# Kernel tuning notes

Hardware: AMD Instinct MI355X
Metric: run time of the kernel (lower is better)

## Reference

```python
import jax, jax.numpy as jnp
import numpy as np

jax.config.update("jax_enable_x64", True)  # int64 coordinate hashes (scaling up to 1e15)

N_IN, N_OUT = 64, 32
NP_, NG = 200000, 400000

# Same coordinate hash as the original module: columns [batch, x, y, z]
_SCALE = jnp.array([1, 10 ** 5, 10 ** 10, 10 ** 15], dtype=jnp.int64)
# 27 kernel offsets of the 3x3x3 generative transpose conv (output-stride units)
_OFF3 = np.array([[i, j, k] for i in (-1, 0, 1) for j in (-1, 0, 1) for k in (-1, 0, 1)], dtype=np.int64)
_OFF4 = jnp.asarray(np.concatenate([np.zeros((27, 1), np.int64), _OFF3], axis=1))  # batch offset = 0


def _hash(c):
    return (c.astype(jnp.int64) * _SCALE).sum(-1)


def setup_inputs() -> dict:
    rng = np.random.default_rng(0)
    G = 128  # stride-2 lattice: input coords are even, in [0, 256)
    lin = rng.choice(G ** 3, size=NP_, replace=False)  # unique voxels
    xs, ys, zs = lin % G, (lin // G) % G, lin // (G * G)
    in_coords = np.stack([np.zeros(NP_, np.int64), 2 * xs, 2 * ys, 2 * zs], axis=1)
    # guide (occupied) coords: input coords shifted by random kernel offsets -> mostly hits
    guide_coords = np.concatenate([in_coords, in_coords], axis=0).copy()
    guide_coords[:, 1:] += _OFF3[rng.integers(0, 27, size=NG)]
    key = jax.random.key(0)
    k1, k2, k3 = jax.random.split(key, 3)
    in_feats = jax.random.normal(k1, (NP_, N_IN), dtype=jnp.float32)
    weights = (jax.random.normal(k2, (27, N_IN, N_OUT), dtype=jnp.float32) / float(np.sqrt(27 * N_IN))).astype(jnp.float32)
    bias = (jax.random.normal(k3, (N_OUT,), dtype=jnp.float32) * 0.01).astype(jnp.float32)
    return {"in_feats": in_feats, "weights": weights, "bias": bias,
            "in_coords": jnp.asarray(in_coords), "guide_coords": jnp.asarray(guide_coords)}


def _forward(in_feats, weights, bias, in_coords, guide_coords):
    # Hash-table over input coordinates (sort + binary search == isin with index)
    in_keys = _hash(in_coords)                # [Np]
    order = jnp.argsort(in_keys)
    skeys = in_keys[order]
    n = skeys.shape[0]
    # Generative transpose conv: output q gets contribution from input p when q = p + off,
    # i.e. p = q - off. Pruning keeps only outputs coinciding with guide coords, so we
    # evaluate the conv directly at the guide coordinates and mask non-generated rows.
    p_keys = _hash(guide_coords[None, :, :] - _OFF4[:, None, :])   # [27, Ng]
    pos = jnp.clip(jnp.searchsorted(skeys, p_keys), 0, n - 1)
    found = skeys[pos] == p_keys                                   # [27, Ng] bool
    idx = order[pos]                                               # [27, Ng]

    def step(acc, xs):
        i, f, w = xs
        g = in_feats[i] * f[:, None].astype(in_feats.dtype)        # [Ng, N_in] gather + mask
        return acc + g @ w, None                                   # small GEMM per offset

    acc0 = jnp.zeros((guide_coords.shape[0], weights.shape[-1]), in_feats.dtype)
    acc, _ = jax.lax.scan(step, acc0, (idx, found, weights))
    exists = found.any(axis=0)                                     # generated-set membership
    return (acc + bias.astype(acc.dtype)) * exists[:, None].astype(acc.dtype)


def reference(in_feats, weights, bias, in_coords, guide_coords):
    return _forward(in_feats, weights, bias, in_coords, guide_coords)
```

## Files before the change

kernel.cpp:

```cpp
#include <hip/hip_runtime.h>

#define NIN 64
#define NOUT 32
#define TBITS 21
#define TSIZE (1 << TBITS)
#define NB 512
#define CHUNK 4096
#define KPT (CHUNK / 256)
#define BLKG 128

typedef __attribute__((ext_vector_type(8))) short short8;
typedef __attribute__((ext_vector_type(4))) float float4v;
typedef __attribute__((ext_vector_type(4))) unsigned short ushort4v;

__device__ __forceinline__ unsigned short bf16rne(float x) {
    unsigned u = __float_as_uint(x);
    u += 0x7fffu + ((u >> 16) & 1u);
    return (unsigned short)(u >> 16);
}

__device__ __forceinline__ int bucket_of(int4 q, int* cls) {
    int c = (q.y & 1) | ((q.z & 1) << 1) | ((q.w & 1) << 2);
    *cls = c;
    int sp = ((q.y >> 6) & 3) | (((q.z >> 6) & 3) << 2) | (((q.w >> 6) & 3) << 4);
    return (c << 6) | sp;
}

__global__ void prep(int4* __restrict__ ws4, int n4,
                     int4* __restrict__ count4,
                     const float* __restrict__ w, unsigned short* __restrict__ wt,
                     const float* __restrict__ f, unsigned short* __restrict__ fb,
                     int fn4) {
    int i = blockIdx.x * blockDim.x + threadIdx.x;
    if (i < n4) ws4[i] = make_int4(-1, -1, -1, -1);
    if (i < NB / 4) count4[i] = make_int4(0, 0, 0, 0);
    if (i < 27 * 64 * 32) {
        int oi = i >> 11;
        int k  = (i >> 5) & 63;
        int ch = i & 31;
        wt[oi * 2048 + ch * 64 + k] = bf16rne(w[i]);
    }
    if (i < fn4) {
        float4 v = ((const float4*)f)[i];
        ushort4v o;
        o.x = bf16rne(v.x); o.y = bf16rne(v.y);
        o.z = bf16rne(v.z); o.w = bf16rne(v.w);
        ((ushort4v*)fb)[i] = o;
    }
}

__global__ void bc(const int* __restrict__ coords, int np, int* __restrict__ table,
                   const int* __restrict__ guide, int ng, int* __restrict__ count) {
    __shared__ int hist[NB];
    for (int i = threadIdx.x; i < NB; i += blockDim.x) hist[i] = 0;
    int gi = blockIdx.x * blockDim.x + threadIdx.x;
    if (gi < np) {
        int x = coords[gi * 4 + 1];
        int y = coords[gi * 4 + 2];
        int z = coords[gi * 4 + 3];
        table[(x >> 1) | ((y >> 1) << 7) | ((z >> 1) << 14)] = gi;
    }
    __syncthreads();
    int base = blockIdx.x * CHUNK;
    if (base < ng) {
        int end = base + CHUNK; if (end > ng) end = ng;
        for (int i = base + threadIdx.x; i < end; i += blockDim.x) {
            int c;
            int b = bucket_of(((const int4*)guide)[i], &c);
            atomicAdd(&hist[b], 1);
        }
        __syncthreads();
        for (int i = threadIdx.x; i < NB; i += blockDim.x)
            if (hist[i]) atomicAdd(&count[i], hist[i]);
    }
}

__global__ void scanB(const int* __restrict__ count, int* __restrict__ cursor,
                      int* __restrict__ classbase) {
    __shared__ int ps[512];
    __shared__ int cb[9];
    int t = threadIdx.x;
    int v = count[t];
    ps[t] = v;
    __syncthreads();
    #pragma unroll
    for (int off = 1; off < 512; off <<= 1) {
        int val = ps[t];
        int u = (t >= off) ? ps[t - off] : 0;
        __syncthreads();
        ps[t] = val + u;
        __syncthreads();
    }
    int incl = ps[t];
    if (t == 0) {
        int base = 0;
        #pragma unroll
        for (int cc = 0; cc < 8; ++cc) {
            cb[cc] = base;
            int hi = ps[cc * 64 + 63];
            int lo = cc ? ps[cc * 64 - 1] : 0;
            base += (hi - lo + BLKG - 1) & ~(BLKG - 1);
        }
        cb[8] = base;
        for (int j = 0; j < 9; ++j) classbase[j] = cb[j];
    }
    __syncthreads();
    int cc = t >> 6;
    int lo = cc ? ps[cc * 64 - 1] : 0;
    cursor[t] = cb[cc] + (incl - v) - lo;
}

__global__ void scat(const int* __restrict__ guide, int ng,
                     int* __restrict__ cursor, int2* __restrict__ sorted) {
    __shared__ int hist[NB];
    int t = threadIdx.x;
    for (int i = t; i < NB; i += 256) hist[i] = 0;
    __syncthreads();
    int base = blockIdx.x * CHUNK;
    int packed[KPT];
    int ey[KPT];
    #pragma unroll
    for (int k = 0; k < KPT; ++k) {
        int i = base + k * 256 + t;
        packed[k] = -1;
        ey[k] = 0;
        if (i < ng) {
            int4 q = ((const int4*)guide)[i];
            int c;
            int b = bucket_of(q, &c);
            int lr = atomicAdd(&hist[b], 1);
            packed[k] = (b << 13) | lr;
            ey[k] = (q.y + 1) | ((q.z + 1) << 9) | ((q.w + 1) << 18);
        }
    }
    __syncthreads();
    for (int i = t; i < NB; i += 256) {
        int h = hist[i];
        hist[i] = h ? atomicAdd(&cursor[i], h) : 0;
    }
    __syncthreads();
    #pragma unroll
    for (int k = 0; k < KPT; ++k) {
        if (packed[k] >= 0) {
            int b  = packed[k] >> 13;
            int lr = packed[k] & 8191;
            int i  = base + k * 256 + t;
            int2 e;
            e.x = i | ((b >> 6) << 24);
            e.y = ey[k];
            sorted[hist[b] + lr] = e;
        }
    }
}


template<int C>
__device__ __forceinline__ void probe2t(const int* __restrict__ table, int2 s2,
                                        int quad, int* o0, int* o1) {
    int qx = (s2.y & 511) - 1;
    int qy = ((s2.y >> 9) & 511) - 1;
    int qz = ((s2.y >> 18) & 511) - 1;
    int res[2];
    #pragma unroll
    for (int r = 0; r < 2; ++r) {
        int sub = quad + r * 4;
        int offx = (C & 1) ? ((sub & 1) ? 1 : -1) : 0;
        int offy = (C & 2) ? ((sub & 2) ? 1 : -1) : 0;
        int offz = (C & 4) ? ((sub & 4) ? 1 : -1) : 0;
        int px = qx - offx, py = qy - offy, pz = qz - offz;
        bool valid = (s2.x >= 0) & ((sub & ~C & 7) == 0) &
                     ((unsigned)px < 256u) & ((unsigned)py < 256u) & ((unsigned)pz < 256u);
        int lin = (px >> 1) | ((py >> 1) << 7) | ((pz >> 1) << 14);
        int v = table[valid ? lin : 0];
        res[r] = valid ? v : -1;
    }
    *o0 = res[0]; *o1 = res[1];
}

template<int C, int SUB>
__device__ __forceinline__ void stage_sub(const unsigned short* __restrict__ wt,
                                          unsigned short* bshr, int m, int j) {
    if constexpr ((SUB & ~C & 7) == 0) {
        constexpr int offx = (C & 1) ? ((SUB & 1) ? 1 : -1) : 0;
        constexpr int offy = (C & 2) ? ((SUB & 2) ? 1 : -1) : 0;
        constexpr int offz = (C & 4) ? ((SUB & 4) ? 1 : -1) : 0;
        constexpr int oi = (offx + 1) * 9 + (offy + 1) * 3 + (offz + 1);
        short8 v = *(const short8*)(wt + oi * 2048 + m * 64 + j * 8);
        *(short8*)((char*)bshr + SUB * 4096 + m * 128 + ((j ^ (m & 7)) << 4)) = v;
    }
}

template<int USEFB, int C, int SUB>
__device__ __forceinline__ void slot_load(const float* __restrict__ feats,
                                          const unsigned short* __restrict__ fb,
                                          int idx0, int idx1,
                                          unsigned long long bal0, unsigned long long bal1,
                                          int m, int quad, short8* A0, short8* A1) {
    if constexpr ((SUB & ~C & 7) == 0) {
        unsigned long long bal = (SUB < 4) ? bal0 : bal1;
        unsigned rowm = (unsigned)((bal >> ((SUB & 3) * 16)) & 0xffffull);
        short8 z = {0,0,0,0,0,0,0,0};
        A0[SUB] = z; A1[SUB] = z;
        if (rowm) {
            int h = __shfl((SUB < 4) ? idx0 : idx1, (SUB & 3) * 16 + m, 64);
            if (h >= 0) {
                if constexpr (USEFB) {
                    const unsigned short* fp = fb + (size_t)h * NIN + quad * 8;
                    A0[SUB] = *(const short8*)fp;
                    A1[SUB] = *(const short8*)(fp + 32);
                } else {
                    const float4* fp = (const float4*)(feats + (size_t)h * NIN + quad * 8);
                    float4 fA = fp[0], fB = fp[1];
                    const float4* fp2 = (const float4*)(feats + (size_t)h * NIN + 32 + quad * 8);
                    float4 fC = fp2[0], fD = fp2[1];
                    short8 x, y;
                    x[0] = (short)bf16rne(fA.x); x[1] = (short)bf16rne(fA.y);
                    x[2] = (short)bf16rne(fA.z); x[3] = (short)bf16rne(fA.w);
                    x[4] = (short)bf16rne(fB.x); x[5] = (short)bf16rne(fB.y);
                    x[6] = (short)bf16rne(fB.z); x[7] = (short)bf16rne(fB.w);
                    y[0] = (short)bf16rne(fC.x); y[1] = (short)bf16rne(fC.y);
                    y[2] = (short)bf16rne(fC.z); y[3] = (short)bf16rne(fC.w);
                    y[4] = (short)bf16rne(fD.x); y[5] = (short)bf16rne(fD.y);
                    y[6] = (short)bf16rne(fD.z); y[7] = (short)bf16rne(fD.w);
                    A0[SUB] = x; A1[SUB] = y;
                }
            }
        }
    }
}

template<int C, int SUB>
__device__ __forceinline__ void slot_mm(const unsigned short* bshr,
                                        unsigned long long bal0, unsigned long long bal1,
                                        int m, int quad, const short8* A0, const short8* A1,
                                        float4v* acc0, float4v* acc1) {
    if constexpr ((SUB & ~C & 7) == 0) {
        unsigned long long bal = (SUB < 4) ? bal0 : bal1;
        unsigned rowm = (unsigned)((bal >> ((SUB & 3) * 16)) & 0xffffull);
        if (rowm) {
            const char* base = (const char*)bshr + SUB * 4096;
            short8 b00 = *(const short8*)(base + m * 128 + ((quad ^ (m & 7)) << 4));
            short8 b10 = *(const short8*)(base + m * 128 + (((4 + quad) ^ (m & 7)) << 4));
            short8 b01 = *(const short8*)(base + (16 + m) * 128 + ((quad ^ ((16 + m) & 7)) << 4));
            short8 b11 = *(const short8*)(base + (16 + m) * 128 + (((4 + quad) ^ ((16 + m) & 7)) << 4));
            *acc0 = __builtin_amdgcn_mfma_f32_16x16x32_bf16(A0[SUB], b00, *acc0, 0, 0, 0);
            *acc0 = __builtin_amdgcn_mfma_f32_16x16x32_bf16(A1[SUB], b10, *acc0, 0, 0, 0);
            *acc1 = __builtin_amdgcn_mfma_f32_16x16x32_bf16(A0[SUB], b01, *acc1, 0, 0, 0);
            *acc1 = __builtin_amdgcn_mfma_f32_16x16x32_bf16(A1[SUB], b11, *acc1, 0, 0, 0);
        }
    }
}

template<int USEFB, int C>
__device__ __forceinline__ void conv_class(const float* __restrict__ feats,
                                           const unsigned short* __restrict__ fb,
                                           const float* __restrict__ bias,
                                           const int* __restrict__ table,
                                           const int2* __restrict__ sorted,
                                           const unsigned short* __restrict__ wt,
                                           float* __restrict__ out,
                                           int bt0, unsigned short* bshr) {
    int tid = threadIdx.x;
    {
        int mm = tid >> 3, jj = tid & 7;
        stage_sub<C, 0>(wt, bshr, mm, jj);
        stage_sub<C, 1>(wt, bshr, mm, jj);
        stage_sub<C, 2>(wt, bshr, mm, jj);
        stage_sub<C, 3>(wt, bshr, mm, jj);
        stage_sub<C, 4>(wt, bshr, mm, jj);
        stage_sub<C, 5>(wt, bshr, mm, jj);
        stage_sub<C, 6>(wt, bshr, mm, jj);
        stage_sub<C, 7>(wt, bshr, mm, jj);
    }
    __syncthreads();

    int wid = tid >> 6, lane = tid & 63;
    int m = lane & 15, quad = lane >> 4;
    float bv0 = bias[m], bv1 = bias[16 + m];

    int t0 = bt0 + wid * 2;
    int2 s2 = sorted[t0 * 16 + m];
    int idx0, idx1;
    probe2t<C>(table, s2, quad, &idx0, &idx1);

    #pragma unroll
    for (int tt = 0; tt < 2; ++tt) {
        int t = t0 + tt;
        bool more = (tt == 0);
        int2 s2n = s2;
        if (more) s2n = sorted[(t + 1) * 16 + m];

        int id = (s2.x < 0) ? -1 : (s2.x & 0xffffff);
        unsigned long long bal0 = __ballot(idx0 >= 0);
        unsigned long long bal1 = __ballot(idx1 >= 0);

        float4v acc0 = {0.f, 0.f, 0.f, 0.f};
        float4v acc1 = {0.f, 0.f, 0.f, 0.f};
        short8 A0[8], A1[8];

        slot_load<USEFB, C, 0>(feats, fb, idx0, idx1, bal0, bal1, m, quad, A0, A1);
        slot_load<USEFB, C, 1>(feats, fb, idx0, idx1, bal0, bal1, m, quad, A0, A1);
        slot_load<USEFB, C, 2>(feats, fb, idx0, idx1, bal0, bal1, m, quad, A0, A1);
        slot_load<USEFB, C, 3>(feats, fb, idx0, idx1, bal0, bal1, m, quad, A0, A1);
        slot_mm<C, 0>(bshr, bal0, bal1, m, quad, A0, A1, &acc0, &acc1);
        slot_mm<C, 1>(bshr, bal0, bal1, m, quad, A0, A1, &acc0, &acc1);
        slot_mm<C, 2>(bshr, bal0, bal1, m, quad, A0, A1, &acc0, &acc1);
        slot_mm<C, 3>(bshr, bal0, bal1, m, quad, A0, A1, &acc0, &acc1);
        slot_load<USEFB, C, 4>(feats, fb, idx0, idx1, bal0, bal1, m, quad, A0, A1);
        slot_load<USEFB, C, 5>(feats, fb, idx0, idx1, bal0, bal1, m, quad, A0, A1);
        slot_load<USEFB, C, 6>(feats, fb, idx0, idx1, bal0, bal1, m, quad, A0, A1);
        slot_load<USEFB, C, 7>(feats, fb, idx0, idx1, bal0, bal1, m, quad, A0, A1);
        slot_mm<C, 4>(bshr, bal0, bal1, m, quad, A0, A1, &acc0, &acc1);
        slot_mm<C, 5>(bshr, bal0, bal1, m, quad, A0, A1, &acc0, &acc1);
        slot_mm<C, 6>(bshr, bal0, bal1, m, quad, A0, A1, &acc0, &acc1);
        slot_mm<C, 7>(bshr, bal0, bal1, m, quad, A0, A1, &acc0, &acc1);

        int nidx0 = idx0, nidx1 = idx1;
        if (more) probe2t<C>(table, s2n, quad, &nidx0, &nidx1);

        unsigned long long eb = bal0 | bal1;
        unsigned e16 = (unsigned)((eb | (eb >> 16) | (eb >> 32) | (eb >> 48)) & 0xffffull);
        #pragma unroll
        for (int r = 0; r < 4; ++r) {
            int mr = quad * 4 + r;
            int idr = __shfl(id, mr, 64);
            if (idr >= 0) {
                bool exr = (e16 >> mr) & 1;
                out[(size_t)idr * NOUT + m]      = exr ? (acc0[r] + bv0) : 0.f;
                out[(size_t)idr * NOUT + 16 + m] = exr ? (acc1[r] + bv1) : 0.f;
            }
        }

        s2 = s2n; idx0 = nidx0; idx1 = nidx1;
    }
}

template<int USEFB>
__launch_bounds__(256, 4)
__global__ void gen_conv(const float* __restrict__ feats,
                         const unsigned short* __restrict__ fb,
                         const float* __restrict__ bias,
                         const int* __restrict__ table,
                         const int2* __restrict__ sorted,
                         const int* __restrict__ classbase,
                         const unsigned short* __restrict__ wt,
                         float* __restrict__ out) {
    __shared__ unsigned short bshr[16384];

    int nwg = gridDim.x;
    int orig = blockIdx.x;
    int qd = nwg >> 3, rd = nwg & 7;
    int xc = orig & 7, ix = orig >> 3;
    int wg = (xc < rd ? xc * (qd + 1) : rd * (qd + 1) + (xc - rd) * qd) + ix;

    int g0 = wg * BLKG;
    if (g0 >= classbase[8]) return;
    int c = 0;
    #pragma unroll
    for (int j = 1; j < 8; ++j) c += (g0 >= classbase[j]) ? 1 : 0;
    c = __builtin_amdgcn_readfirstlane(c);
    int bt0 = wg * (BLKG / 16);

    switch (c) {
        case 0: conv_class<USEFB, 0>(feats, fb, bias, table, sorted, wt, out, bt0, bshr); break;
        case 1: conv_class<USEFB, 1>(feats, fb, bias, table, sorted, wt, out, bt0, bshr); break;
        case 2: conv_class<USEFB, 2>(feats, fb, bias, table, sorted, wt, out, bt0, bshr); break;
        case 3: conv_class<USEFB, 3>(feats, fb, bias, table, sorted, wt, out, bt0, bshr); break;
        case 4: conv_class<USEFB, 4>(feats, fb, bias, table, sorted, wt, out, bt0, bshr); break;
        case 5: conv_class<USEFB, 5>(feats, fb, bias, table, sorted, wt, out, bt0, bshr); break;
        case 6: conv_class<USEFB, 6>(feats, fb, bias, table, sorted, wt, out, bt0, bshr); break;
        case 7: conv_class<USEFB, 7>(feats, fb, bias, table, sorted, wt, out, bt0, bshr); break;
    }
}

extern "C" void kernel_launch(void* const* d_in, const int* in_sizes, int n_in,
                              void* d_out, int out_size, void* d_ws, size_t ws_size,
                              hipStream_t stream) {
    const float* feats   = (const float*)d_in[0];
    const float* weights = (const float*)d_in[1];
    const float* bias    = (const float*)d_in[2];
    const int*   coords  = (const int*)d_in[3];
    const int*   guide   = (const int*)d_in[4];
    float* out = (float*)d_out;

    int np = in_sizes[3] / 4;
    int ng = in_sizes[4] / 4;

    int* wsI = (int*)d_ws;
    int SC = (ng + 8 * BLKG + 3) & ~3;
    int A = TSIZE + 2 * SC;
    int* table     = wsI;
    int2* sorted   = (int2*)(wsI + TSIZE);
    int* count     = wsI + A;
    int* cursor    = wsI + A + 512;
    int* classbase = wsI + A + 1024;
    unsigned short* wt = (unsigned short*)(wsI + A + 1040);
    unsigned short* fb = (unsigned short*)(wsI + A + 1040 + 27648);
    size_t need = ((size_t)A + 1040 + 27648) * 4 + (size_t)np * NIN * 2;
    int usefb = (ws_size >= need) ? 1 : 0;

    int n4 = A / 4;
    int fn4 = usefb ? np * (NIN / 4) : 0;
    int prep_n = n4 > fn4 ? n4 : fn4;
    if (prep_n < 27 * 64 * 32) prep_n = 27 * 64 * 32;
    hipLaunchKernelGGL(prep, dim3((prep_n + 255) / 256), dim3(256), 0, stream,
                       (int4*)wsI, n4, (int4*)count, weights, wt, feats, fb, fn4);

    int bcb1 = (np + 255) / 256;
    int bcb2 = (ng + CHUNK - 1) / CHUNK;
    int bc_blocks = bcb1 > bcb2 ? bcb1 : bcb2;
    hipLaunchKernelGGL(bc, dim3(bc_blocks), dim3(256), 0, stream,
                       coords, np, table, guide, ng, count);

    hipLaunchKernelGGL(scanB, dim3(1), dim3(512), 0, stream, count, cursor, classbase);

    hipLaunchKernelGGL(scat, dim3((ng + CHUNK - 1) / CHUNK), dim3(256), 0, stream,
                       guide, ng, cursor, sorted);

    int maxguides = ng + 8 * (BLKG - 1);
    int blocks = (maxguides + BLKG - 1) / BLKG;
    if (usefb) {
        hipLaunchKernelGGL((gen_conv<1>), dim3(blocks), dim3(256), 0, stream,
                           feats, fb, bias, table, sorted, classbase, wt, out);
    } else {
        hipLaunchKernelGGL((gen_conv<0>), dim3(blocks), dim3(256), 0, stream,
                           feats, fb, bias, table, sorted, classbase, wt, out);
    }
}
```

Before: 178.1 us.

## Halve weight LDS staging in two phases, fuse histogram into prep, table into scatter

The conv kernel now stages only four offset weight slices at a time, using 8 KB of shared memory instead of 16 KB. It processes both 16-row tiles together per phase, re-staging for classes with eight offsets, and raises the launch-bounds occupancy hint from 4 to 6. The guide histogram moves into the prep kernel and the input hash-table build moves into the scatter kernel, which removes the separate bc launch. The count reset becomes a memset. The trade-off is extra barriers and a second weight staging pass for eight-offset classes, plus tighter register limits from the higher occupancy target.

```diff
diff --git a/kernel.cpp b/kernel.cpp
--- a/kernel.cpp
+++ b/kernel.cpp
@@ -19,6 +19,14 @@
     return (unsigned short)(u >> 16);
 }
 
+constexpr int popc8(int x) { int n = 0; for (int i = 0; i < 8; ++i) n += (x >> i) & 1; return n; }
+constexpr int nth_sub(int C, int r) {
+    int cnt = 0;
+    for (int s = 0; s < 8; ++s)
+        if ((s & ~C & 7) == 0) { if (cnt == r) return s; ++cnt; }
+    return 0;
+}
+
 __device__ __forceinline__ int bucket_of(int4 q, int* cls) {
     int c = (q.y & 1) | ((q.z & 1) << 1) | ((q.w & 1) << 2);
     *cls = c;
@@ -27,13 +35,13 @@
 }
 
 __global__ void prep(int4* __restrict__ ws4, int n4,
-                     int4* __restrict__ count4,
                      const float* __restrict__ w, unsigned short* __restrict__ wt,
                      const float* __restrict__ f, unsigned short* __restrict__ fb,
-                     int fn4) {
+                     int fn4,
+                     const int* __restrict__ guide, int ng, int* __restrict__ count) {
+    __shared__ int hist[NB];
     int i = blockIdx.x * blockDim.x + threadIdx.x;
     if (i < n4) ws4[i] = make_int4(-1, -1, -1, -1);
-    if (i < NB / 4) count4[i] = make_int4(0, 0, 0, 0);
     if (i < 27 * 64 * 32) {
         int oi = i >> 11;
         int k  = (i >> 5) & 63;
@@ -47,31 +55,19 @@
         o.z = bf16rne(v.z); o.w = bf16rne(v.w);
         ((ushort4v*)fb)[i] = o;
     }
-}
-
-__global__ void bc(const int* __restrict__ coords, int np, int* __restrict__ table,
-                   const int* __restrict__ guide, int ng, int* __restrict__ count) {
-    __shared__ int hist[NB];
-    for (int i = threadIdx.x; i < NB; i += blockDim.x) hist[i] = 0;
-    int gi = blockIdx.x * blockDim.x + threadIdx.x;
-    if (gi < np) {
-        int x = coords[gi * 4 + 1];
-        int y = coords[gi * 4 + 2];
-        int z = coords[gi * 4 + 3];
-        table[(x >> 1) | ((y >> 1) << 7) | ((z >> 1) << 14)] = gi;
-    }
-    __syncthreads();
     int base = blockIdx.x * CHUNK;
     if (base < ng) {
+        for (int j = threadIdx.x; j < NB; j += 256) hist[j] = 0;
+        __syncthreads();
         int end = base + CHUNK; if (end > ng) end = ng;
-        for (int i = base + threadIdx.x; i < end; i += blockDim.x) {
+        for (int j = base + threadIdx.x; j < end; j += 256) {
             int c;
-            int b = bucket_of(((const int4*)guide)[i], &c);
+            int b = bucket_of(((const int4*)guide)[j], &c);
             atomicAdd(&hist[b], 1);
         }
         __syncthreads();
-        for (int i = threadIdx.x; i < NB; i += blockDim.x)
-            if (hist[i]) atomicAdd(&count[i], hist[i]);
+        for (int j = threadIdx.x; j < NB; j += 256)
+            if (hist[j]) atomicAdd(&count[j], hist[j]);
     }
 }
 
@@ -110,13 +106,22 @@
     cursor[t] = cb[cc] + (incl - v) - lo;
 }
 
-__global__ void scat(const int* __restrict__ guide, int ng,
+__global__ void scat(const int* __restrict__ coords, int np, int* __restrict__ table,
+                     const int* __restrict__ guide, int ng,
                      int* __restrict__ cursor, int2* __restrict__ sorted) {
+    int gi = blockIdx.x * blockDim.x + threadIdx.x;
+    if (gi < np) {
+        int x = coords[gi * 4 + 1];
+        int y = coords[gi * 4 + 2];
+        int z = coords[gi * 4 + 3];
+        table[(x >> 1) | ((y >> 1) << 7) | ((z >> 1) << 14)] = gi;
+    }
     __shared__ int hist[NB];
     int t = threadIdx.x;
+    int base = blockIdx.x * CHUNK;
+    if (base >= ng) return;
     for (int i = t; i < NB; i += 256) hist[i] = 0;
     __syncthreads();
-    int base = blockIdx.x * CHUNK;
     int packed[KPT];
     int ey[KPT];
     #pragma unroll
@@ -177,37 +182,39 @@
     *o0 = res[0]; *o1 = res[1];
 }
 
-template<int C, int SUB>
-__device__ __forceinline__ void stage_sub(const unsigned short* __restrict__ wt,
-                                          unsigned short* bshr, int m, int j) {
-    if constexpr ((SUB & ~C & 7) == 0) {
+template<int C, int R, int NS>
+__device__ __forceinline__ void stage_rank(const unsigned short* __restrict__ wt,
+                                           unsigned short* bshr, int mm, int jj) {
+    if constexpr (R < NS) {
+        constexpr int SUB = nth_sub(C, R);
         constexpr int offx = (C & 1) ? ((SUB & 1) ? 1 : -1) : 0;
         constexpr int offy = (C & 2) ? ((SUB & 2) ? 1 : -1) : 0;
         constexpr int offz = (C & 4) ? ((SUB & 4) ? 1 : -1) : 0;
         constexpr int oi = (offx + 1) * 9 + (offy + 1) * 3 + (offz + 1);
-        short8 v = *(const short8*)(wt + oi * 2048 + m * 64 + j * 8);
-        *(short8*)((char*)bshr + SUB * 4096 + m * 128 + ((j ^ (m & 7)) << 4)) = v;
-    }
-}
-
-template<int USEFB, int C, int SUB>
-__device__ __forceinline__ void slot_load(const float* __restrict__ feats,
+        short8 v = *(const short8*)(wt + oi * 2048 + mm * 64 + jj * 8);
+        *(short8*)((char*)bshr + (R & 3) * 4096 + mm * 128 + ((jj ^ (mm & 7)) << 4)) = v;
+    }
+}
+
+template<int USEFB, int C, int R, int NS>
+__device__ __forceinline__ void rank_load(const float* __restrict__ feats,
                                           const unsigned short* __restrict__ fb,
                                           int idx0, int idx1,
                                           unsigned long long bal0, unsigned long long bal1,
                                           int m, int quad, short8* A0, short8* A1) {
-    if constexpr ((SUB & ~C & 7) == 0) {
+    if constexpr (R < NS) {
+        constexpr int SUB = nth_sub(C, R);
         unsigned long long bal = (SUB < 4) ? bal0 : bal1;
         unsigned rowm = (unsigned)((bal >> ((SUB & 3) * 16)) & 0xffffull);
         short8 z = {0,0,0,0,0,0,0,0};
-        A0[SUB] = z; A1[SUB] = z;
+        A0[R & 3] = z; A1[R & 3] = z;
         if (rowm) {
             int h = __shfl((SUB < 4) ? idx0 : idx1, (SUB & 3) * 16 + m, 64);
             if (h >= 0) {
                 if constexpr (USEFB) {
                     const unsigned short* fp = fb + (size_t)h * NIN + quad * 8;
-                    A0[SUB] = *(const short8*)fp;
-                    A1[SUB] = *(const short8*)(fp + 32);
+                    A0[R & 3] = *(const short8*)fp;
+                    A1[R & 3] = *(const short8*)(fp + 32);
                 } else {
                     const float4* fp = (const float4*)(feats + (size_t)h * NIN + quad * 8);
                     float4 fA = fp[0], fB = fp[1];
@@ -222,31 +229,69 @@
                     y[2] = (short)bf16rne(fC.z); y[3] = (short)bf16rne(fC.w);
                     y[4] = (short)bf16rne(fD.x); y[5] = (short)bf16rne(fD.y);
                     y[6] = (short)bf16rne(fD.z); y[7] = (short)bf16rne(fD.w);
-                    A0[SUB] = x; A1[SUB] = y;
+                    A0[R & 3] = x; A1[R & 3] = y;
                 }
             }
         }
     }
 }
 
-template<int C, int SUB>
-__device__ __forceinline__ void slot_mm(const unsigned short* bshr,
+template<int C, int R, int NS>
+__device__ __forceinline__ void rank_mm(const unsigned short* bshr,
                                         unsigned long long bal0, unsigned long long bal1,
                                         int m, int quad, const short8* A0, const short8* A1,
                                         float4v* acc0, float4v* acc1) {
-    if constexpr ((SUB & ~C & 7) == 0) {
+    if constexpr (R < NS) {
+        constexpr int SUB = nth_sub(C, R);
         unsigned long long bal = (SUB < 4) ? bal0 : bal1;
         unsigned rowm = (unsigned)((bal >> ((SUB & 3) * 16)) & 0xffffull);
         if (rowm) {
-            const char* base = (const char*)bshr + SUB * 4096;
+            const char* base = (const char*)bshr + (R & 3) * 4096;
             short8 b00 = *(const short8*)(base + m * 128 + ((quad ^ (m & 7)) << 4));
             short8 b10 = *(const short8*)(base + m * 128 + (((4 + quad) ^ (m & 7)) << 4));
             short8 b01 = *(const short8*)(base + (16 + m) * 128 + ((quad ^ ((16 + m) & 7)) << 4));
             short8 b11 = *(const short8*)(base + (16 + m) * 128 + (((4 + quad) ^ ((16 + m) & 7)) << 4));
-            *acc0 = __builtin_amdgcn_mfma_f32_16x16x32_bf16(A0[SUB], b00, *acc0, 0, 0, 0);
-            *acc0 = __builtin_amdgcn_mfma_f32_16x16x32_bf16(A1[SUB], b10, *acc0, 0, 0, 0);
-            *acc1 = __builtin_amdgcn_mfma_f32_16x16x32_bf16(A0[SUB], b01, *acc1, 0, 0, 0);
-            *acc1 = __builtin_amdgcn_mfma_f32_16x16x32_bf16(A1[SUB], b11, *acc1, 0, 0, 0);
+            *acc0 = __builtin_amdgcn_mfma_f32_16x16x32_bf16(A0[R & 3], b00, *acc0, 0, 0, 0);
+            *acc0 = __builtin_amdgcn_mfma_f32_16x16x32_bf16(A1[R & 3], b10, *acc0, 0, 0, 0);
+            *acc1 = __builtin_amdgcn_mfma_f32_16x16x32_bf16(A0[R & 3], b01, *acc1, 0, 0, 0);
+            *acc1 = __builtin_amdgcn_mfma_f32_16x16x32_bf16(A1[R & 3], b11, *acc1, 0, 0, 0);
+        }
+    }
+}
+
+template<int USEFB, int C, int P>
+__device__ __forceinline__ void phase_tile(const float* __restrict__ feats,
+                                           const unsigned short* __restrict__ fb,
+                                           const unsigned short* bshr,
+                                           int idx0, int idx1,
+                                           unsigned long long bal0, unsigned long long bal1,
+                                           int m, int quad, float4v* acc0, float4v* acc1) {
+    constexpr int NS = 1 << popc8(C);
+    short8 A0[4], A1[4];
+    rank_load<USEFB, C, P * 4 + 0, NS>(feats, fb, idx0, idx1, bal0, bal1, m, quad, A0, A1);
+    rank_load<USEFB, C, P * 4 + 1, NS>(feats, fb, idx0, idx1, bal0, bal1, m, quad, A0, A1);
+    rank_load<USEFB, C, P * 4 + 2, NS>(feats, fb, idx0, idx1, bal0, bal1, m, quad, A0, A1);
+    rank_load<USEFB, C, P * 4 + 3, NS>(feats, fb, idx0, idx1, bal0, bal1, m, quad, A0, A1);
+    rank_mm<C, P * 4 + 0, NS>(bshr, bal0, bal1, m, quad, A0, A1, acc0, acc1);
+    rank_mm<C, P * 4 + 1, NS>(bshr, bal0, bal1, m, quad, A0, A1, acc0, acc1);
+    rank_mm<C, P * 4 + 2, NS>(bshr, bal0, bal1, m, quad, A0, A1, acc0, acc1);
+    rank_mm<C, P * 4 + 3, NS>(bshr, bal0, bal1, m, quad, A0, A1, acc0, acc1);
+}
+
+__device__ __forceinline__ void store_tile(int2 s2, unsigned long long eb,
+                                           float4v acc0, float4v acc1,
+                                           int m, int quad, float bv0, float bv1,
+                                           float* __restrict__ out) {
+    int id = (s2.x < 0) ? -1 : (s2.x & 0xffffff);
+    unsigned e16 = (unsigned)((eb | (eb >> 16) | (eb >> 32) | (eb >> 48)) & 0xffffull);
+    #pragma unroll
+    for (int r = 0; r < 4; ++r) {
+        int mr = quad * 4 + r;
+        int idr = __shfl(id, mr, 64);
+        if (idr >= 0) {
+            bool exr = (e16 >> mr) & 1;
+            out[(size_t)idr * NOUT + m]      = exr ? (acc0[r] + bv0) : 0.f;
+            out[(size_t)idr * NOUT + 16 + m] = exr ? (acc1[r] + bv1) : 0.f;
         }
     }
 }
@@ -260,83 +305,57 @@
                                            const unsigned short* __restrict__ wt,
                                            float* __restrict__ out,
                                            int bt0, unsigned short* bshr) {
+    constexpr int NS = 1 << popc8(C);
     int tid = threadIdx.x;
-    {
-        int mm = tid >> 3, jj = tid & 7;
-        stage_sub<C, 0>(wt, bshr, mm, jj);
-        stage_sub<C, 1>(wt, bshr, mm, jj);
-        stage_sub<C, 2>(wt, bshr, mm, jj);
-        stage_sub<C, 3>(wt, bshr, mm, jj);
-        stage_sub<C, 4>(wt, bshr, mm, jj);
-        stage_sub<C, 5>(wt, bshr, mm, jj);
-        stage_sub<C, 6>(wt, bshr, mm, jj);
-        stage_sub<C, 7>(wt, bshr, mm, jj);
-    }
-    __syncthreads();
-
     int wid = tid >> 6, lane = tid & 63;
     int m = lane & 15, quad = lane >> 4;
     float bv0 = bias[m], bv1 = bias[16 + m];
 
     int t0 = bt0 + wid * 2;
-    int2 s2 = sorted[t0 * 16 + m];
-    int idx0, idx1;
-    probe2t<C>(table, s2, quad, &idx0, &idx1);
-
-    #pragma unroll
-    for (int tt = 0; tt < 2; ++tt) {
-        int t = t0 + tt;
-        bool more = (tt == 0);
-        int2 s2n = s2;
-        if (more) s2n = sorted[(t + 1) * 16 + m];
-
-        int id = (s2.x < 0) ? -1 : (s2.x & 0xffffff);
-        unsigned long long bal0 = __ballot(idx0 >= 0);
-        unsigned long long bal1 = __ballot(idx1 >= 0);
-
-        float4v acc0 = {0.f, 0.f, 0.f, 0.f};
-        float4v acc1 = {0.f, 0.f, 0.f, 0.f};
-        short8 A0[8], A1[8];
-
-        slot_load<USEFB, C, 0>(feats, fb, idx0, idx1, bal0, bal1, m, quad, A0, A1);
-        slot_load<USEFB, C, 1>(feats, fb, idx0, idx1, bal0, bal1, m, quad, A0, A1);
-        slot_load<USEFB, C, 2>(feats, fb, idx0, idx1, bal0, bal1, m, quad, A0, A1);
-        slot_load<USEFB, C, 3>(feats, fb, idx0, idx1, bal0, bal1, m, quad, A0, A1);
-        slot_mm<C, 0>(bshr, bal0, bal1, m, quad, A0, A1, &acc0, &acc1);
-        slot_mm<C, 1>(bshr, bal0, bal1, m, quad, A0, A1, &acc0, &acc1);
-        slot_mm<C, 2>(bshr, bal0, bal1, m, quad, A0, A1, &acc0, &acc1);
-        slot_mm<C, 3>(bshr, bal0, bal1, m, quad, A0, A1, &acc0, &acc1);
-        slot_load<USEFB, C, 4>(feats, fb, idx0, idx1, bal0, bal1, m, quad, A0, A1);
-        slot_load<USEFB, C, 5>(feats, fb, idx0, idx1, bal0, bal1, m, quad, A0, A1);
-        slot_load<USEFB, C, 6>(feats, fb, idx0, idx1, bal0, bal1, m, quad, A0, A1);
-        slot_load<USEFB, C, 7>(feats, fb, idx0, idx1, bal0, bal1, m, quad, A0, A1);
-        slot_mm<C, 4>(bshr, bal0, bal1, m, quad, A0, A1, &acc0, &acc1);
-        slot_mm<C, 5>(bshr, bal0, bal1, m, quad, A0, A1, &acc0, &acc1);
-        slot_mm<C, 6>(bshr, bal0, bal1, m, quad, A0, A1, &acc0, &acc1);
-        slot_mm<C, 7>(bshr, bal0, bal1, m, quad, A0, A1, &acc0, &acc1);
-
-        int nidx0 = idx0, nidx1 = idx1;
-        if (more) probe2t<C>(table, s2n, quad, &nidx0, &nidx1);
-
-        unsigned long long eb = bal0 | bal1;
-        unsigned e16 = (unsigned)((eb | (eb >> 16) | (eb >> 32) | (eb >> 48)) & 0xffffull);
-        #pragma unroll
-        for (int r = 0; r < 4; ++r) {
-            int mr = quad * 4 + r;
-            int idr = __shfl(id, mr, 64);
-            if (idr >= 0) {
-                bool exr = (e16 >> mr) & 1;
-                out[(size_t)idr * NOUT + m]      = exr ? (acc0[r] + bv0) : 0.f;
-                out[(size_t)idr * NOUT + 16 + m] = exr ? (acc1[r] + bv1) : 0.f;
-            }
-        }
-
-        s2 = s2n; idx0 = nidx0; idx1 = nidx1;
-    }
+    int2 s2a = sorted[t0 * 16 + m];
+    int2 s2b = sorted[t0 * 16 + 16 + m];
+    int ia0, ia1, ib0, ib1;
+    probe2t<C>(table, s2a, quad, &ia0, &ia1);
+    probe2t<C>(table, s2b, quad, &ib0, &ib1);
+
+    {
+        int mm = tid >> 3, jj = tid & 7;
+        stage_rank<C, 0, NS>(wt, bshr, mm, jj);
+        stage_rank<C, 1, NS>(wt, bshr, mm, jj);
+        stage_rank<C, 2, NS>(wt, bshr, mm, jj);
+        stage_rank<C, 3, NS>(wt, bshr, mm, jj);
+    }
+    __syncthreads();
+
+    unsigned long long balA0 = __ballot(ia0 >= 0), balA1 = __ballot(ia1 >= 0);
+    unsigned long long balB0 = __ballot(ib0 >= 0), balB1 = __ballot(ib1 >= 0);
+
+    float4v aA0 = {0.f,0.f,0.f,0.f}, aA1 = {0.f,0.f,0.f,0.f};
+    float4v aB0 = {0.f,0.f,0.f,0.f}, aB1 = {0.f,0.f,0.f,0.f};
+
+    phase_tile<USEFB, C, 0>(feats, fb, bshr, ia0, ia1, balA0, balA1, m, quad, &aA0, &aA1);
+    phase_tile<USEFB, C, 0>(feats, fb, bshr, ib0, ib1, balB0, balB1, m, quad, &aB0, &aB1);
+
+    if constexpr (NS > 4) {
+        __syncthreads();
+        {
+            int mm = tid >> 3, jj = tid & 7;
+            stage_rank<C, 4, NS>(wt, bshr, mm, jj);
+            stage_rank<C, 5, NS>(wt, bshr, mm, jj);
+            stage_rank<C, 6, NS>(wt, bshr, mm, jj);
+            stage_rank<C, 7, NS>(wt, bshr, mm, jj);
+        }
+        __syncthreads();
+        phase_tile<USEFB, C, 1>(feats, fb, bshr, ia0, ia1, balA0, balA1, m, quad, &aA0, &aA1);
+        phase_tile<USEFB, C, 1>(feats, fb, bshr, ib0, ib1, balB0, balB1, m, quad, &aB0, &aB1);
+    }
+
+    store_tile(s2a, balA0 | balA1, aA0, aA1, m, quad, bv0, bv1, out);
+    store_tile(s2b, balB0 | balB1, aB0, aB1, m, quad, bv0, bv1, out);
 }
 
 template<int USEFB>
-__launch_bounds__(256, 4)
+__launch_bounds__(256, 6)
 __global__ void gen_conv(const float* __restrict__ feats,
                          const unsigned short* __restrict__ fb,
                          const float* __restrict__ bias,
@@ -345,7 +364,7 @@
                          const int* __restrict__ classbase,
                          const unsigned short* __restrict__ wt,
                          float* __restrict__ out) {
-    __shared__ unsigned short bshr[16384];
+    __shared__ unsigned short bshr[8192];
 
     int nwg = gridDim.x;
     int orig = blockIdx.x;
@@ -399,23 +418,24 @@
     size_t need = ((size_t)A + 1040 + 27648) * 4 + (size_t)np * NIN * 2;
     int usefb = (ws_size >= need) ? 1 : 0;
 
+    hipMemsetAsync(count, 0, NB * sizeof(int), stream);
+
     int n4 = A / 4;
     int fn4 = usefb ? np * (NIN / 4) : 0;
     int prep_n = n4 > fn4 ? n4 : fn4;
     if (prep_n < 27 * 64 * 32) prep_n = 27 * 64 * 32;
-    hipLaunchKernelGGL(prep, dim3((prep_n + 255) / 256), dim3(256), 0, stream,
-                       (int4*)wsI, n4, (int4*)count, weights, wt, feats, fb, fn4);
-
-    int bcb1 = (np + 255) / 256;
-    int bcb2 = (ng + CHUNK - 1) / CHUNK;
-    int bc_blocks = bcb1 > bcb2 ? bcb1 : bcb2;
-    hipLaunchKernelGGL(bc, dim3(bc_blocks), dim3(256), 0, stream,
-                       coords, np, table, guide, ng, count);
+    int prep_blocks = (prep_n + 255) / 256;
+    int cblocks = (ng + CHUNK - 1) / CHUNK;
+    if (prep_blocks < cblocks) prep_blocks = cblocks;
+    hipLaunchKernelGGL(prep, dim3(prep_blocks), dim3(256), 0, stream,
+                       (int4*)wsI, n4, weights, wt, feats, fb, fn4, guide, ng, count);
 
     hipLaunchKernelGGL(scanB, dim3(1), dim3(512), 0, stream, count, cursor, classbase);
 
-    hipLaunchKernelGGL(scat, dim3((ng + CHUNK - 1) / CHUNK), dim3(256), 0, stream,
-                       guide, ng, cursor, sorted);
+    int sb1 = (np + 255) / 256;
+    int sblocks = sb1 > cblocks ? sb1 : cblocks;
+    hipLaunchKernelGGL(scat, dim3(sblocks), dim3(256), 0, stream,
+                       coords, np, table, guide, ng, cursor, sorted);
 
     int maxguides = ng + 8 * (BLKG - 1);
     int blocks = (maxguides + BLKG - 1) / BLKG;
```

Result: faster. 172.1 us (-3.4%).
